# Kernel tuning notes

Measured on AMD Instinct MI355X. Metric: run time of the kernel, lower is better.

Reference implementation:

```python
import jax, jax.numpy as jnp
import numpy as np

EPS_LN = 1e-5
EPS_SUMNORM = 1e-5
B, T, F, H = 8, 1024, 128, 64


def setup_inputs() -> dict:
    key = jax.random.key(0)
    ks = jax.random.split(key, 12)
    s = lambda fan_in: 1.0 / np.sqrt(fan_in)
    inp = {
        "x": jax.random.normal(ks[0], (B, T, F), dtype=jnp.float32),
        "state": jax.random.normal(ks[1], (B, 1, H * H), dtype=jnp.float32),
        # nn.Linear weights are [out, in]
        "Wk": jax.random.uniform(ks[2], (H, F), minval=-s(F), maxval=s(F)),
        "Wq": jax.random.uniform(ks[3], (H, F), minval=-s(F), maxval=s(F)),
        "Wv": jax.random.uniform(ks[4], (H, F), minval=-s(F), maxval=s(F)),
        "gamma": jnp.ones((F,), dtype=jnp.float32),
        "beta": jnp.zeros((F,), dtype=jnp.float32),
        "W1": jax.random.uniform(ks[5], (H, H), minval=-s(H), maxval=s(H)),
        "b1": jax.random.uniform(ks[6], (H,), minval=-s(H), maxval=s(H)),
        "W2": jax.random.uniform(ks[7], (H, H), minval=-s(H), maxval=s(H)),
        "b2": jax.random.uniform(ks[8], (H,), minval=-s(H), maxval=s(H)),
        "Ws": jax.random.uniform(ks[9], (H, F), minval=-s(F), maxval=s(F)),
        "bs": jax.random.uniform(ks[10], (H,), minval=-s(F), maxval=s(F)),
    }
    return inp


def reference(x, state, Wk, Wq, Wv, gamma, beta, W1, b1, W2, b2, Ws, bs):
    # LayerNorm over feature dim
    mu = jnp.mean(x, axis=-1, keepdims=True)
    var = jnp.var(x, axis=-1, keepdims=True)
    xn = (x - mu) * jax.lax.rsqrt(var + EPS_LN) * gamma + beta  # [B,T,F]

    K = jax.nn.relu(jnp.einsum('btf,hf->bth', xn, Wk))
    Q = jax.nn.relu(jnp.einsum('btf,hf->bth', xn, Wq))
    V = jnp.einsum('btf,hf->bth', xn, Wv)

    # sum normalization
    K = K / (EPS_SUMNORM + jnp.sum(K, axis=-1, keepdims=True))
    Q = Q / (EPS_SUMNORM + jnp.sum(Q, axis=-1, keepdims=True))

    # outer-product fast weights: kv[b,t,i,j] = V[b,t,i] * K[b,t,j]
    kv = jnp.einsum('bti,btj->btij', V, K)  # [B,T,H,H]

    # 'sum' aggregator: running sum over time starting from initial state
    S = jnp.cumsum(kv, axis=1) + state.reshape(B, 1, H, H)  # [B,T,H,H]

    y = jnp.einsum('btij,btj->bti', S, Q)  # [B,T,H]

    # feed forward
    y = jax.nn.relu(jnp.einsum('bti,oi->bto', y, W1) + b1)
    y = jax.nn.relu(jnp.einsum('bti,oi->bto', y, W2) + b2)

    # residual shortcut (from the normalized x, matching the torch reassignment)
    y = y + jnp.einsum('btf,hf->bth', xn, Ws) + bs
    return y, S
```

## Files before the change

### kernel.cpp

```cpp
#include <hip/hip_runtime.h>

#define Bn 8
#define Tn 1024
#define Fn 128
#define Hn 64
#define NC 32
#define CSZ 32

constexpr float EPS = 1e-5f;

__device__ __forceinline__ void fma4(float4& a, float s, const float4& w) {
    a.x = fmaf(s, w.x, a.x); a.y = fmaf(s, w.y, a.y);
    a.z = fmaf(s, w.z, a.z); a.w = fmaf(s, w.w, a.w);
}
__device__ __forceinline__ float4 f4zero() { return make_float4(0.f, 0.f, 0.f, 0.f); }

__global__ __launch_bounds__(256) void k_ln(const float* __restrict__ x,
                                            const float* __restrict__ gamma,
                                            const float* __restrict__ beta,
                                            float* __restrict__ xn) {
    const int w = threadIdx.x >> 6, lane = threadIdx.x & 63;
    const int tok = blockIdx.x * 4 + w;
    const float2 xv = *(const float2*)(x + tok * Fn + lane * 2);
    float s  = xv.x + xv.y;
    float ss = xv.x * xv.x + xv.y * xv.y;
#pragma unroll
    for (int m = 1; m < 64; m <<= 1) { s += __shfl_xor(s, m); ss += __shfl_xor(ss, m); }
    const float mu  = s * (1.0f / Fn);
    const float var = ss * (1.0f / Fn) - mu * mu;
    const float rs  = rsqrtf(var + EPS);
    const float2 g  = *(const float2*)(gamma + lane * 2);
    const float2 bt = *(const float2*)(beta + lane * 2);
    float2 o;
    o.x = (xv.x - mu) * rs * g.x + bt.x;
    o.y = (xv.y - mu) * rs * g.y + bt.y;
    *(float2*)(xn + tok * Fn + lane * 2) = o;
}

__global__ __launch_bounds__(256) void k_proj(const float* __restrict__ xn,
                                              const float* __restrict__ Wk,
                                              const float* __restrict__ Wq,
                                              const float* __restrict__ Wv,
                                              const float* __restrict__ Wsp,
                                              const float* __restrict__ bs,
                                              float* __restrict__ Kb, float* __restrict__ Qb,
                                              float* __restrict__ Vb, float* __restrict__ Rb) {
    __shared__ float LW[32 * 260];
    __shared__ float LX[32 * 36];
    const int tid  = threadIdx.x;
    const int tok0 = blockIdx.x * 32;
    const int tg   = tid >> 6;
    const int cg   = tid & 63;

    const int   ms   = tid >> 6;
    const float* WmS = (ms == 0) ? Wk : (ms == 1) ? Wq : (ms == 2) ? Wv : Wsp;
    const float* wrow = WmS + (tid & 63) * Fn;

    float4 acc[8];
#pragma unroll
    for (int i = 0; i < 8; i++) acc[i] = f4zero();

    for (int kc0 = 0; kc0 < Fn; kc0 += 32) {
#pragma unroll
        for (int r = 0; r < 8; r++) {
            const float4 wv = *(const float4*)(wrow + kc0 + r * 4);
            LW[(r * 4 + 0) * 260 + tid] = wv.x;
            LW[(r * 4 + 1) * 260 + tid] = wv.y;
            LW[(r * 4 + 2) * 260 + tid] = wv.z;
            LW[(r * 4 + 3) * 260 + tid] = wv.w;
        }
        {
            const int tt = tid >> 3, kk = (tid & 7) * 4;
            const float4 xv = *(const float4*)(xn + (tok0 + tt) * Fn + kc0 + kk);
            LX[(kk + 0) * 36 + tt] = xv.x;
            LX[(kk + 1) * 36 + tt] = xv.y;
            LX[(kk + 2) * 36 + tt] = xv.z;
            LX[(kk + 3) * 36 + tt] = xv.w;
        }
        __syncthreads();
#pragma unroll 8
        for (int kc = 0; kc < 32; kc++) {
            const float4 w4 = *(const float4*)&LW[kc * 260 + cg * 4];
            const float4 xa = *(const float4*)&LX[kc * 36 + tg * 8];
            const float4 xb = *(const float4*)&LX[kc * 36 + tg * 8 + 4];
            fma4(acc[0], xa.x, w4); fma4(acc[1], xa.y, w4);
            fma4(acc[2], xa.z, w4); fma4(acc[3], xa.w, w4);
            fma4(acc[4], xb.x, w4); fma4(acc[5], xb.y, w4);
            fma4(acc[6], xb.z, w4); fma4(acc[7], xb.w, w4);
        }
        __syncthreads();
    }
    const int m  = cg >> 4;
    const int h0 = (cg & 15) * 4;
    float* outp = (m == 0) ? Kb : (m == 1) ? Qb : (m == 2) ? Vb : Rb;
    if (m < 2) {
#pragma unroll
        for (int i = 0; i < 8; i++) {
            acc[i].x = fmaxf(acc[i].x, 0.f); acc[i].y = fmaxf(acc[i].y, 0.f);
            acc[i].z = fmaxf(acc[i].z, 0.f); acc[i].w = fmaxf(acc[i].w, 0.f);
        }
    } else if (m == 3) {
        const float4 bv = *(const float4*)(bs + h0);
#pragma unroll
        for (int i = 0; i < 8; i++) {
            acc[i].x += bv.x; acc[i].y += bv.y; acc[i].z += bv.z; acc[i].w += bv.w;
        }
    }
#pragma unroll
    for (int ti = 0; ti < 8; ti++)
        *(float4*)(outp + (tok0 + tg * 8 + ti) * Hn + h0) = acc[ti];
}

__global__ __launch_bounds__(256) void k_sumnorm(float* __restrict__ Kb, float* __restrict__ Qb) {
    const int w = threadIdx.x >> 6, lane = threadIdx.x & 63;
    const int tok = blockIdx.x * 2 + (w & 1);
    float* buf = (w >> 1) ? Qb : Kb;
    const float v = buf[tok * Hn + lane];
    float s = v;
#pragma unroll
    for (int m = 1; m < 64; m <<= 1) s += __shfl_xor(s, m);
    buf[tok * Hn + lane] = v / (EPS + s);
}

__global__ __launch_bounds__(256) void k_csum(const float* __restrict__ Kb,
                                              const float* __restrict__ Vb,
                                              float* __restrict__ csum) {
    __shared__ float Kc[CSZ * Hn];
    __shared__ float Vc[CSZ * Hn];
    const int tid = threadIdx.x;
    const int b = blockIdx.x >> 5, c = blockIdx.x & 31;
    const int t0 = c * CSZ;
    const float4* Kg = (const float4*)(Kb + (b * Tn + t0) * Hn);
    const float4* Vg = (const float4*)(Vb + (b * Tn + t0) * Hn);
#pragma unroll
    for (int r = 0; r < 2; r++) {
        ((float4*)Kc)[tid + 256 * r] = Kg[tid + 256 * r];
        ((float4*)Vc)[tid + 256 * r] = Vg[tid + 256 * r];
    }
    __syncthreads();
    float4 acc[4];
#pragma unroll
    for (int s = 0; s < 4; s++) acc[s] = f4zero();
    const int jq = tid & 15, rr = tid >> 4;
    for (int t = 0; t < CSZ; t++) {
        const float4 kv = ((const float4*)Kc)[t * 16 + jq];
#pragma unroll
        for (int s = 0; s < 4; s++) {
            const float v = Vc[t * Hn + s * 16 + rr];
            fma4(acc[s], v, kv);
        }
    }
    float4* out = (float4*)(csum + (size_t)(b * NC + c) * Hn * Hn);
#pragma unroll
    for (int s = 0; s < 4; s++) out[s * 256 + tid] = acc[s];
}

__global__ __launch_bounds__(256) void k_scan(const float* __restrict__ state,
                                              const float* __restrict__ csum,
                                              float* __restrict__ cstart) {
    const int b = blockIdx.x >> 4, et = blockIdx.x & 15;
    const int e = et * 256 + threadIdx.x;
    float v[NC];
#pragma unroll
    for (int c = 0; c < NC; c++) v[c] = csum[(size_t)(b * NC + c) * 4096 + e];
    float acc = state[b * 4096 + e];
#pragma unroll
    for (int c = 0; c < NC; c++) {
        cstart[(size_t)(b * NC + c) * 4096 + e] = acc;
        acc += v[c];
    }
}

__global__ __launch_bounds__(256) void k_main(const float* __restrict__ Kb,
                                              const float* __restrict__ Qb,
                                              const float* __restrict__ Vb,
                                              const float* __restrict__ cstart,
                                              float* __restrict__ yraw,
                                              float* __restrict__ outS) {
    __shared__ float Kc[CSZ * Hn];
    __shared__ float Qc[CSZ * Hn];
    __shared__ float Vc[CSZ * Hn];
    const int tid = threadIdx.x;
    const int b = blockIdx.x >> 5, c = blockIdx.x & 31;
    const int t0 = c * CSZ;
    const float4* Kg = (const float4*)(Kb + (b * Tn + t0) * Hn);
    const float4* Qg = (const float4*)(Qb + (b * Tn + t0) * Hn);
    const float4* Vg = (const float4*)(Vb + (b * Tn + t0) * Hn);
#pragma unroll
    for (int r = 0; r < 2; r++) {
        ((float4*)Kc)[tid + 256 * r] = Kg[tid + 256 * r];
        ((float4*)Qc)[tid + 256 * r] = Qg[tid + 256 * r];
        ((float4*)Vc)[tid + 256 * r] = Vg[tid + 256 * r];
    }
    float4 S4[4];
    const float4* cs = (const float4*)(cstart + (size_t)(b * NC + c) * 4096);
#pragma unroll
    for (int s = 0; s < 4; s++) S4[s] = cs[s * 256 + tid];
    __syncthreads();
    const int jq = tid & 15, rr = tid >> 4;
    float* yBase = yraw + (b * Tn + t0) * Hn;
    float4* SBase = (float4*)outS + (size_t)(b * Tn + t0) * 1024;
    for (int t = 0; t < CSZ; t++) {
        const float4 kv = ((const float4*)Kc)[t * 16 + jq];
        const float4 qv = ((const float4*)Qc)[t * 16 + jq];
        float yp[4];
#pragma unroll
        for (int s = 0; s < 4; s++) {
            const float v = Vc[t * Hn + s * 16 + rr];
            fma4(S4[s], v, kv);
            yp[s] = S4[s].x * qv.x + S4[s].y * qv.y + S4[s].z * qv.z + S4[s].w * qv.w;
        }
        float4* So = SBase + t * 1024;
#pragma unroll
        for (int s = 0; s < 4; s++) So[s * 256 + tid] = S4[s];
#pragma unroll
        for (int s = 0; s < 4; s++) {
            yp[s] += __shfl_xor(yp[s], 1);
            yp[s] += __shfl_xor(yp[s], 2);
            yp[s] += __shfl_xor(yp[s], 4);
            yp[s] += __shfl_xor(yp[s], 8);
        }
        if (jq == 0) {
#pragma unroll
            for (int s = 0; s < 4; s++) yBase[t * Hn + s * 16 + rr] = yp[s];
        }
    }
}

__global__ __launch_bounds__(256) void k_ffn(const float* __restrict__ yraw,
                                             const float* __restrict__ W1,
                                             const float* __restrict__ b1,
                                             const float* __restrict__ W2,
                                             const float* __restrict__ b2,
                                             const float* __restrict__ Rb,
                                             float* __restrict__ outY) {
    __shared__ float WT[2][64 * 68];
    __shared__ float Yt[64 * 36];
    __shared__ float Y2[64 * 36];
    __shared__ float Lb[2][64];
    const int tid = threadIdx.x;
    const int tok0 = blockIdx.x * 32;
    for (int mat = 0; mat < 2; mat++) {
        const float4* Wg = (const float4*)(mat ? W2 : W1);
#pragma unroll
        for (int r = 0; r < 4; r++) {
            const int f4i = tid + 256 * r;
            const float4 wv = Wg[f4i];
            const int h = f4i >> 4;
            const int k = (f4i & 15) * 4;
            WT[mat][(k + 0) * 68 + h] = wv.x;
            WT[mat][(k + 1) * 68 + h] = wv.y;
            WT[mat][(k + 2) * 68 + h] = wv.z;
            WT[mat][(k + 3) * 68 + h] = wv.w;
        }
    }
    if (tid < 64) Lb[0][tid] = b1[tid];
    else if (tid < 128) Lb[1][tid - 64] = b2[tid - 64];
    {
        const float4* Yg = (const float4*)(yraw + tok0 * Hn);
#pragma unroll
        for (int r = 0; r < 2; r++) {
            const int f4i = tid + 256 * r;
            const float4 yv = Yg[f4i];
            const int tok = f4i >> 4;
            const int k = (f4i & 15) * 4;
            Yt[(k + 0) * 36 + tok] = yv.x;
            Yt[(k + 1) * 36 + tok] = yv.y;
            Yt[(k + 2) * 36 + tok] = yv.z;
            Yt[(k + 3) * 36 + tok] = yv.w;
        }
    }
    __syncthreads();
    const int tg = tid >> 4, cg = tid & 15;
    float4 a0 = f4zero(), a1 = f4zero();
#pragma unroll 16
    for (int k = 0; k < 64; k++) {
        const float2 y2 = *(const float2*)&Yt[k * 36 + tg * 2];
        const float4 w4 = *(const float4*)&WT[0][k * 68 + cg * 4];
        fma4(a0, y2.x, w4); fma4(a1, y2.y, w4);
    }
    {
        const float4 bv = *(const float4*)&Lb[0][cg * 4];
        a0.x = fmaxf(a0.x + bv.x, 0.f); a0.y = fmaxf(a0.y + bv.y, 0.f);
        a0.z = fmaxf(a0.z + bv.z, 0.f); a0.w = fmaxf(a0.w + bv.w, 0.f);
        a1.x = fmaxf(a1.x + bv.x, 0.f); a1.y = fmaxf(a1.y + bv.y, 0.f);
        a1.z = fmaxf(a1.z + bv.z, 0.f); a1.w = fmaxf(a1.w + bv.w, 0.f);
    }
    Y2[(cg * 4 + 0) * 36 + tg * 2] = a0.x;
    Y2[(cg * 4 + 1) * 36 + tg * 2] = a0.y;
    Y2[(cg * 4 + 2) * 36 + tg * 2] = a0.z;
    Y2[(cg * 4 + 3) * 36 + tg * 2] = a0.w;
    Y2[(cg * 4 + 0) * 36 + tg * 2 + 1] = a1.x;
    Y2[(cg * 4 + 1) * 36 + tg * 2 + 1] = a1.y;
    Y2[(cg * 4 + 2) * 36 + tg * 2 + 1] = a1.z;
    Y2[(cg * 4 + 3) * 36 + tg * 2 + 1] = a1.w;
    __syncthreads();
    float4 c0 = f4zero(), c1 = f4zero();
#pragma unroll 16
    for (int k = 0; k < 64; k++) {
        const float2 y2 = *(const float2*)&Y2[k * 36 + tg * 2];
        const float4 w4 = *(const float4*)&WT[1][k * 68 + cg * 4];
        fma4(c0, y2.x, w4); fma4(c1, y2.y, w4);
    }
    const int tokA = tok0 + tg * 2, tokB = tokA + 1;
    const float4 bv = *(const float4*)&Lb[1][cg * 4];
    const float4 r0 = *(const float4*)(Rb + tokA * Hn + cg * 4);
    const float4 r1 = *(const float4*)(Rb + tokB * Hn + cg * 4);
    float4 o0, o1;
    o0.x = fmaxf(c0.x + bv.x, 0.f) + r0.x; o0.y = fmaxf(c0.y + bv.y, 0.f) + r0.y;
    o0.z = fmaxf(c0.z + bv.z, 0.f) + r0.z; o0.w = fmaxf(c0.w + bv.w, 0.f) + r0.w;
    o1.x = fmaxf(c1.x + bv.x, 0.f) + r1.x; o1.y = fmaxf(c1.y + bv.y, 0.f) + r1.y;
    o1.z = fmaxf(c1.z + bv.z, 0.f) + r1.z; o1.w = fmaxf(c1.w + bv.w, 0.f) + r1.w;
    *(float4*)(outY + tokA * Hn + cg * 4) = o0;
    *(float4*)(outY + tokB * Hn + cg * 4) = o1;
}

extern "C" void kernel_launch(void* const* d_in, const int* in_sizes, int n_in,
                              void* d_out, int out_size, void* d_ws, size_t ws_size,
                              hipStream_t stream) {
    const float* x     = (const float*)d_in[0];
    const float* state = (const float*)d_in[1];
    const float* Wk    = (const float*)d_in[2];
    const float* Wq    = (const float*)d_in[3];
    const float* Wv    = (const float*)d_in[4];
    const float* gamma = (const float*)d_in[5];
    const float* beta  = (const float*)d_in[6];
    const float* W1    = (const float*)d_in[7];
    const float* b1    = (const float*)d_in[8];
    const float* W2    = (const float*)d_in[9];
    const float* b2    = (const float*)d_in[10];
    const float* Wsp   = (const float*)d_in[11];
    const float* bs    = (const float*)d_in[12];

    float* ws     = (float*)d_ws;
    float* Kb     = ws;
    float* Qb     = ws + 524288;
    float* Vb     = ws + 1048576;
    float* Rb     = ws + 1572864;
    float* yraw   = ws + 2097152;
    float* csum   = ws + 2621440;
    float* cstart = ws + 3670016;
    float* xn     = ws + 4718592;

    float* outY = (float*)d_out;
    float* outS = outY + (size_t)Bn * Tn * Hn;

    k_ln<<<2048, 256, 0, stream>>>(x, gamma, beta, xn);
    k_proj<<<256, 256, 0, stream>>>(xn, Wk, Wq, Wv, Wsp, bs, Kb, Qb, Vb, Rb);
    k_sumnorm<<<4096, 256, 0, stream>>>(Kb, Qb);
    k_csum<<<256, 256, 0, stream>>>(Kb, Vb, csum);
    k_scan<<<128, 256, 0, stream>>>(state, csum, cstart);
    k_main<<<256, 256, 0, stream>>>(Kb, Qb, Vb, cstart, yraw, outS);
    k_ffn<<<256, 256, 0, stream>>>(yraw, W1, b1, W2, b2, Rb, outY);
}
```

Measured before the change: 208.3 us.

## Fuse LayerNorm, sumnorm and chunk sums into projection; fuse FFN into scan-main

Reduces seven kernels to three. LayerNorm is computed in registers inside the projection kernel, and the sum-normalisation and per-chunk KV outer-product sums are folded into its epilogue. The FFN is merged into the main recurrence kernel. Chunk size halves to 16 so the main kernel launches 512 blocks, and the scan writes chunk starts in place. This removes the xn, yraw and cstart round trips and several launches, at the cost of a larger per-thread register array in the scan (64 chunks) and heavier per-block work.

```diff
diff --git a/kernel.cpp b/kernel.cpp
--- a/kernel.cpp
+++ b/kernel.cpp
@@ -4,8 +4,8 @@
 #define Tn 1024
 #define Fn 128
 #define Hn 64
-#define NC 32
-#define CSZ 32
+#define NC 64
+#define CSZ 16
 
 constexpr float EPS = 1e-5f;
 
@@ -15,52 +15,45 @@
 }
 __device__ __forceinline__ float4 f4zero() { return make_float4(0.f, 0.f, 0.f, 0.f); }
 
-__global__ __launch_bounds__(256) void k_ln(const float* __restrict__ x,
-                                            const float* __restrict__ gamma,
-                                            const float* __restrict__ beta,
-                                            float* __restrict__ xn) {
-    const int w = threadIdx.x >> 6, lane = threadIdx.x & 63;
-    const int tok = blockIdx.x * 4 + w;
-    const float2 xv = *(const float2*)(x + tok * Fn + lane * 2);
-    float s  = xv.x + xv.y;
-    float ss = xv.x * xv.x + xv.y * xv.y;
-#pragma unroll
-    for (int m = 1; m < 64; m <<= 1) { s += __shfl_xor(s, m); ss += __shfl_xor(ss, m); }
-    const float mu  = s * (1.0f / Fn);
-    const float var = ss * (1.0f / Fn) - mu * mu;
-    const float rs  = rsqrtf(var + EPS);
-    const float2 g  = *(const float2*)(gamma + lane * 2);
-    const float2 bt = *(const float2*)(beta + lane * 2);
-    float2 o;
-    o.x = (xv.x - mu) * rs * g.x + bt.x;
-    o.y = (xv.y - mu) * rs * g.y + bt.y;
-    *(float2*)(xn + tok * Fn + lane * 2) = o;
-}
-
-__global__ __launch_bounds__(256) void k_proj(const float* __restrict__ xn,
-                                              const float* __restrict__ Wk,
-                                              const float* __restrict__ Wq,
-                                              const float* __restrict__ Wv,
-                                              const float* __restrict__ Wsp,
-                                              const float* __restrict__ bs,
-                                              float* __restrict__ Kb, float* __restrict__ Qb,
-                                              float* __restrict__ Vb, float* __restrict__ Rb) {
+__global__ __launch_bounds__(256) void k1_proj(
+    const float* __restrict__ x, const float* __restrict__ gamma, const float* __restrict__ beta,
+    const float* __restrict__ Wk, const float* __restrict__ Wq, const float* __restrict__ Wv,
+    const float* __restrict__ Wsp, const float* __restrict__ bs,
+    float* __restrict__ Kb, float* __restrict__ Qb, float* __restrict__ Vb, float* __restrict__ Rb,
+    float* __restrict__ csum) {
     __shared__ float LW[32 * 260];
     __shared__ float LX[32 * 36];
+    __shared__ float Kc[32 * Hn];
+    __shared__ float Vc[32 * Hn];
     const int tid  = threadIdx.x;
     const int tok0 = blockIdx.x * 32;
     const int tg   = tid >> 6;
     const int cg   = tid & 63;
 
-    const int   ms   = tid >> 6;
-    const float* WmS = (ms == 0) ? Wk : (ms == 1) ? Wq : (ms == 2) ? Wv : Wsp;
+    const float* WmS  = (tg == 0) ? Wk : (tg == 1) ? Wq : (tg == 2) ? Wv : Wsp;
     const float* wrow = WmS + (tid & 63) * Fn;
 
+    const int tt = tid >> 3, kk = (tid & 7) * 4;
+    float4 xreg[4];
+    float s = 0.f, ss = 0.f;
+#pragma unroll
+    for (int c = 0; c < 4; c++) {
+        xreg[c] = *(const float4*)(x + (tok0 + tt) * Fn + c * 32 + kk);
+        s  += xreg[c].x + xreg[c].y + xreg[c].z + xreg[c].w;
+        ss += xreg[c].x * xreg[c].x + xreg[c].y * xreg[c].y
+            + xreg[c].z * xreg[c].z + xreg[c].w * xreg[c].w;
+    }
+#pragma unroll
+    for (int m = 1; m < 8; m <<= 1) { s += __shfl_xor(s, m); ss += __shfl_xor(ss, m); }
+    const float mu = s * (1.f / Fn);
+    const float rs = rsqrtf(ss * (1.f / Fn) - mu * mu + EPS);
+
     float4 acc[8];
 #pragma unroll
     for (int i = 0; i < 8; i++) acc[i] = f4zero();
 
-    for (int kc0 = 0; kc0 < Fn; kc0 += 32) {
+    for (int c = 0; c < 4; c++) {
+        const int kc0 = c * 32;
 #pragma unroll
         for (int r = 0; r < 8; r++) {
             const float4 wv = *(const float4*)(wrow + kc0 + r * 4);
@@ -70,12 +63,13 @@
             LW[(r * 4 + 3) * 260 + tid] = wv.w;
         }
         {
-            const int tt = tid >> 3, kk = (tid & 7) * 4;
-            const float4 xv = *(const float4*)(xn + (tok0 + tt) * Fn + kc0 + kk);
-            LX[(kk + 0) * 36 + tt] = xv.x;
-            LX[(kk + 1) * 36 + tt] = xv.y;
-            LX[(kk + 2) * 36 + tt] = xv.z;
-            LX[(kk + 3) * 36 + tt] = xv.w;
+            const float4 g4 = *(const float4*)(gamma + kc0 + kk);
+            const float4 b4 = *(const float4*)(beta + kc0 + kk);
+            const float4 xv = xreg[c];
+            LX[(kk + 0) * 36 + tt] = (xv.x - mu) * rs * g4.x + b4.x;
+            LX[(kk + 1) * 36 + tt] = (xv.y - mu) * rs * g4.y + b4.y;
+            LX[(kk + 2) * 36 + tt] = (xv.z - mu) * rs * g4.z + b4.z;
+            LX[(kk + 3) * 36 + tt] = (xv.w - mu) * rs * g4.w + b4.w;
         }
         __syncthreads();
 #pragma unroll 8
@@ -90,15 +84,31 @@
         }
         __syncthreads();
     }
+
     const int m  = cg >> 4;
     const int h0 = (cg & 15) * 4;
-    float* outp = (m == 0) ? Kb : (m == 1) ? Qb : (m == 2) ? Vb : Rb;
     if (m < 2) {
 #pragma unroll
         for (int i = 0; i < 8; i++) {
             acc[i].x = fmaxf(acc[i].x, 0.f); acc[i].y = fmaxf(acc[i].y, 0.f);
             acc[i].z = fmaxf(acc[i].z, 0.f); acc[i].w = fmaxf(acc[i].w, 0.f);
         }
+    }
+    float rsum[8];
+#pragma unroll
+    for (int i = 0; i < 8; i++) {
+        rsum[i] = acc[i].x + acc[i].y + acc[i].z + acc[i].w;
+        rsum[i] += __shfl_xor(rsum[i], 1);
+        rsum[i] += __shfl_xor(rsum[i], 2);
+        rsum[i] += __shfl_xor(rsum[i], 4);
+        rsum[i] += __shfl_xor(rsum[i], 8);
+    }
+    if (m < 2) {
+#pragma unroll
+        for (int i = 0; i < 8; i++) {
+            const float inv = 1.f / (EPS + rsum[i]);
+            acc[i].x *= inv; acc[i].y *= inv; acc[i].z *= inv; acc[i].w *= inv;
+        }
     } else if (m == 3) {
         const float4 bv = *(const float4*)(bs + h0);
 #pragma unroll
@@ -106,58 +116,46 @@
             acc[i].x += bv.x; acc[i].y += bv.y; acc[i].z += bv.z; acc[i].w += bv.w;
         }
     }
+    float* outp = (m == 0) ? Kb : (m == 1) ? Qb : (m == 2) ? Vb : Rb;
 #pragma unroll
     for (int ti = 0; ti < 8; ti++)
         *(float4*)(outp + (tok0 + tg * 8 + ti) * Hn + h0) = acc[ti];
-}
-
-__global__ __launch_bounds__(256) void k_sumnorm(float* __restrict__ Kb, float* __restrict__ Qb) {
-    const int w = threadIdx.x >> 6, lane = threadIdx.x & 63;
-    const int tok = blockIdx.x * 2 + (w & 1);
-    float* buf = (w >> 1) ? Qb : Kb;
-    const float v = buf[tok * Hn + lane];
-    float s = v;
-#pragma unroll
-    for (int m = 1; m < 64; m <<= 1) s += __shfl_xor(s, m);
-    buf[tok * Hn + lane] = v / (EPS + s);
-}
-
-__global__ __launch_bounds__(256) void k_csum(const float* __restrict__ Kb,
-                                              const float* __restrict__ Vb,
-                                              float* __restrict__ csum) {
-    __shared__ float Kc[CSZ * Hn];
-    __shared__ float Vc[CSZ * Hn];
-    const int tid = threadIdx.x;
-    const int b = blockIdx.x >> 5, c = blockIdx.x & 31;
-    const int t0 = c * CSZ;
-    const float4* Kg = (const float4*)(Kb + (b * Tn + t0) * Hn);
-    const float4* Vg = (const float4*)(Vb + (b * Tn + t0) * Hn);
-#pragma unroll
-    for (int r = 0; r < 2; r++) {
-        ((float4*)Kc)[tid + 256 * r] = Kg[tid + 256 * r];
-        ((float4*)Vc)[tid + 256 * r] = Vg[tid + 256 * r];
-    }
-    __syncthreads();
-    float4 acc[4];
-#pragma unroll
-    for (int s = 0; s < 4; s++) acc[s] = f4zero();
+    if (m == 0) {
+#pragma unroll
+        for (int ti = 0; ti < 8; ti++) *(float4*)(Kc + (tg * 8 + ti) * Hn + h0) = acc[ti];
+    } else if (m == 2) {
+#pragma unroll
+        for (int ti = 0; ti < 8; ti++) *(float4*)(Vc + (tg * 8 + ti) * Hn + h0) = acc[ti];
+    }
+    __syncthreads();
+
     const int jq = tid & 15, rr = tid >> 4;
-    for (int t = 0; t < CSZ; t++) {
+    const int b  = tok0 >> 10;
+    const int c0 = ((tok0 & 1023) >> 5) * 2;
+    float4 a4[4];
+    float4* out0 = (float4*)(csum + (size_t)(b * NC + c0) * 4096);
+#pragma unroll
+    for (int sI = 0; sI < 4; sI++) a4[sI] = f4zero();
+    for (int t = 0; t < 16; t++) {
         const float4 kv = ((const float4*)Kc)[t * 16 + jq];
 #pragma unroll
-        for (int s = 0; s < 4; s++) {
-            const float v = Vc[t * Hn + s * 16 + rr];
-            fma4(acc[s], v, kv);
-        }
-    }
-    float4* out = (float4*)(csum + (size_t)(b * NC + c) * Hn * Hn);
-#pragma unroll
-    for (int s = 0; s < 4; s++) out[s * 256 + tid] = acc[s];
-}
-
-__global__ __launch_bounds__(256) void k_scan(const float* __restrict__ state,
-                                              const float* __restrict__ csum,
-                                              float* __restrict__ cstart) {
+        for (int sI = 0; sI < 4; sI++) fma4(a4[sI], Vc[t * Hn + sI * 16 + rr], kv);
+    }
+#pragma unroll
+    for (int sI = 0; sI < 4; sI++) out0[sI * 256 + tid] = a4[sI];
+#pragma unroll
+    for (int sI = 0; sI < 4; sI++) a4[sI] = f4zero();
+    for (int t = 16; t < 32; t++) {
+        const float4 kv = ((const float4*)Kc)[t * 16 + jq];
+#pragma unroll
+        for (int sI = 0; sI < 4; sI++) fma4(a4[sI], Vc[t * Hn + sI * 16 + rr], kv);
+    }
+#pragma unroll
+    for (int sI = 0; sI < 4; sI++) out0[1024 + sI * 256 + tid] = a4[sI];
+}
+
+__global__ __launch_bounds__(256) void k2_scan(const float* __restrict__ state,
+                                               float* __restrict__ csum) {
     const int b = blockIdx.x >> 4, et = blockIdx.x & 15;
     const int e = et * 256 + threadIdx.x;
     float v[NC];
@@ -166,80 +164,31 @@
     float acc = state[b * 4096 + e];
 #pragma unroll
     for (int c = 0; c < NC; c++) {
-        cstart[(size_t)(b * NC + c) * 4096 + e] = acc;
+        csum[(size_t)(b * NC + c) * 4096 + e] = acc;
         acc += v[c];
     }
 }
 
-__global__ __launch_bounds__(256) void k_main(const float* __restrict__ Kb,
-                                              const float* __restrict__ Qb,
-                                              const float* __restrict__ Vb,
-                                              const float* __restrict__ cstart,
-                                              float* __restrict__ yraw,
-                                              float* __restrict__ outS) {
+__global__ __launch_bounds__(256, 2) void k3_main(
+    const float* __restrict__ Kb, const float* __restrict__ Qb, const float* __restrict__ Vb,
+    const float* __restrict__ cstart, const float* __restrict__ Rb,
+    const float* __restrict__ W1, const float* __restrict__ b1,
+    const float* __restrict__ W2, const float* __restrict__ b2,
+    float* __restrict__ outY, float* __restrict__ outS) {
     __shared__ float Kc[CSZ * Hn];
     __shared__ float Qc[CSZ * Hn];
     __shared__ float Vc[CSZ * Hn];
-    const int tid = threadIdx.x;
-    const int b = blockIdx.x >> 5, c = blockIdx.x & 31;
-    const int t0 = c * CSZ;
-    const float4* Kg = (const float4*)(Kb + (b * Tn + t0) * Hn);
-    const float4* Qg = (const float4*)(Qb + (b * Tn + t0) * Hn);
-    const float4* Vg = (const float4*)(Vb + (b * Tn + t0) * Hn);
-#pragma unroll
-    for (int r = 0; r < 2; r++) {
-        ((float4*)Kc)[tid + 256 * r] = Kg[tid + 256 * r];
-        ((float4*)Qc)[tid + 256 * r] = Qg[tid + 256 * r];
-        ((float4*)Vc)[tid + 256 * r] = Vg[tid + 256 * r];
-    }
-    float4 S4[4];
-    const float4* cs = (const float4*)(cstart + (size_t)(b * NC + c) * 4096);
-#pragma unroll
-    for (int s = 0; s < 4; s++) S4[s] = cs[s * 256 + tid];
-    __syncthreads();
-    const int jq = tid & 15, rr = tid >> 4;
-    float* yBase = yraw + (b * Tn + t0) * Hn;
-    float4* SBase = (float4*)outS + (size_t)(b * Tn + t0) * 1024;
-    for (int t = 0; t < CSZ; t++) {
-        const float4 kv = ((const float4*)Kc)[t * 16 + jq];
-        const float4 qv = ((const float4*)Qc)[t * 16 + jq];
-        float yp[4];
-#pragma unroll
-        for (int s = 0; s < 4; s++) {
-            const float v = Vc[t * Hn + s * 16 + rr];
-            fma4(S4[s], v, kv);
-            yp[s] = S4[s].x * qv.x + S4[s].y * qv.y + S4[s].z * qv.z + S4[s].w * qv.w;
-        }
-        float4* So = SBase + t * 1024;
-#pragma unroll
-        for (int s = 0; s < 4; s++) So[s * 256 + tid] = S4[s];
-#pragma unroll
-        for (int s = 0; s < 4; s++) {
-            yp[s] += __shfl_xor(yp[s], 1);
-            yp[s] += __shfl_xor(yp[s], 2);
-            yp[s] += __shfl_xor(yp[s], 4);
-            yp[s] += __shfl_xor(yp[s], 8);
-        }
-        if (jq == 0) {
-#pragma unroll
-            for (int s = 0; s < 4; s++) yBase[t * Hn + s * 16 + rr] = yp[s];
-        }
-    }
-}
-
-__global__ __launch_bounds__(256) void k_ffn(const float* __restrict__ yraw,
-                                             const float* __restrict__ W1,
-                                             const float* __restrict__ b1,
-                                             const float* __restrict__ W2,
-                                             const float* __restrict__ b2,
-                                             const float* __restrict__ Rb,
-                                             float* __restrict__ outY) {
     __shared__ float WT[2][64 * 68];
-    __shared__ float Yt[64 * 36];
-    __shared__ float Y2[64 * 36];
+    __shared__ float Yl[CSZ * 68];
+    __shared__ float Y2[CSZ * 68];
     __shared__ float Lb[2][64];
     const int tid = threadIdx.x;
-    const int tok0 = blockIdx.x * 32;
+    const int b = blockIdx.x >> 6, c = blockIdx.x & 63;
+    const int t0 = c * CSZ;
+    ((float4*)Kc)[tid] = ((const float4*)(Kb + (b * Tn + t0) * Hn))[tid];
+    ((float4*)Qc)[tid] = ((const float4*)(Qb + (b * Tn + t0) * Hn))[tid];
+    ((float4*)Vc)[tid] = ((const float4*)(Vb + (b * Tn + t0) * Hn))[tid];
+#pragma unroll
     for (int mat = 0; mat < 2; mat++) {
         const float4* Wg = (const float4*)(mat ? W2 : W1);
 #pragma unroll
@@ -256,63 +205,56 @@
     }
     if (tid < 64) Lb[0][tid] = b1[tid];
     else if (tid < 128) Lb[1][tid - 64] = b2[tid - 64];
-    {
-        const float4* Yg = (const float4*)(yraw + tok0 * Hn);
-#pragma unroll
-        for (int r = 0; r < 2; r++) {
-            const int f4i = tid + 256 * r;
-            const float4 yv = Yg[f4i];
-            const int tok = f4i >> 4;
-            const int k = (f4i & 15) * 4;
-            Yt[(k + 0) * 36 + tok] = yv.x;
-            Yt[(k + 1) * 36 + tok] = yv.y;
-            Yt[(k + 2) * 36 + tok] = yv.z;
-            Yt[(k + 3) * 36 + tok] = yv.w;
-        }
-    }
-    __syncthreads();
+    float4 S4[4];
+    const float4* cs = (const float4*)(cstart + (size_t)(b * NC + c) * 4096);
+#pragma unroll
+    for (int sI = 0; sI < 4; sI++) S4[sI] = cs[sI * 256 + tid];
+    __syncthreads();
+
+    const int jq = tid & 15, rr = tid >> 4;
+    float4* SBase = (float4*)outS + (size_t)(b * Tn + t0) * 1024;
+    for (int t = 0; t < CSZ; t++) {
+        const float4 kv = ((const float4*)Kc)[t * 16 + jq];
+        const float4 qv = ((const float4*)Qc)[t * 16 + jq];
+        float yp[4];
+#pragma unroll
+        for (int sI = 0; sI < 4; sI++) {
+            fma4(S4[sI], Vc[t * Hn + sI * 16 + rr], kv);
+            yp[sI] = S4[sI].x * qv.x + S4[sI].y * qv.y + S4[sI].z * qv.z + S4[sI].w * qv.w;
+        }
+        float4* So = SBase + t * 1024;
+#pragma unroll
+        for (int sI = 0; sI < 4; sI++) So[sI * 256 + tid] = S4[sI];
+#pragma unroll
+        for (int sI = 0; sI < 4; sI++) {
+            yp[sI] += __shfl_xor(yp[sI], 1);
+            yp[sI] += __shfl_xor(yp[sI], 2);
+            yp[sI] += __shfl_xor(yp[sI], 4);
+            yp[sI] += __shfl_xor(yp[sI], 8);
+        }
+        if (jq == 0) {
+#pragma unroll
+            for (int sI = 0; sI < 4; sI++) Yl[t * 68 + sI * 16 + rr] = yp[sI];
+        }
+    }
+    __syncthreads();
+
     const int tg = tid >> 4, cg = tid & 15;
-    float4 a0 = f4zero(), a1 = f4zero();
+    float4 a = *(const float4*)&Lb[0][cg * 4];
 #pragma unroll 16
-    for (int k = 0; k < 64; k++) {
-        const float2 y2 = *(const float2*)&Yt[k * 36 + tg * 2];
-        const float4 w4 = *(const float4*)&WT[0][k * 68 + cg * 4];
-        fma4(a0, y2.x, w4); fma4(a1, y2.y, w4);
-    }
-    {
-        const float4 bv = *(const float4*)&Lb[0][cg * 4];
-        a0.x = fmaxf(a0.x + bv.x, 0.f); a0.y = fmaxf(a0.y + bv.y, 0.f);
-        a0.z = fmaxf(a0.z + bv.z, 0.f); a0.w = fmaxf(a0.w + bv.w, 0.f);
-        a1.x = fmaxf(a1.x + bv.x, 0.f); a1.y = fmaxf(a1.y + bv.y, 0.f);
-        a1.z = fmaxf(a1.z + bv.z, 0.f); a1.w = fmaxf(a1.w + bv.w, 0.f);
-    }
-    Y2[(cg * 4 + 0) * 36 + tg * 2] = a0.x;
-    Y2[(cg * 4 + 1) * 36 + tg * 2] = a0.y;
-    Y2[(cg * 4 + 2) * 36 + tg * 2] = a0.z;
-    Y2[(cg * 4 + 3) * 36 + tg * 2] = a0.w;
-    Y2[(cg * 4 + 0) * 36 + tg * 2 + 1] = a1.x;
-    Y2[(cg * 4 + 1) * 36 + tg * 2 + 1] = a1.y;
-    Y2[(cg * 4 + 2) * 36 + tg * 2 + 1] = a1.z;
-    Y2[(cg * 4 + 3) * 36 + tg * 2 + 1] = a1.w;
-    __syncthreads();
-    float4 c0 = f4zero(), c1 = f4zero();
+    for (int k = 0; k < 64; k++)
+        fma4(a, Yl[tg * 68 + k], *(const float4*)&WT[0][k * 68 + cg * 4]);
+    a.x = fmaxf(a.x, 0.f); a.y = fmaxf(a.y, 0.f); a.z = fmaxf(a.z, 0.f); a.w = fmaxf(a.w, 0.f);
+    *(float4*)&Y2[tg * 68 + cg * 4] = a;
+    __syncthreads();
+    float4 o = *(const float4*)&Lb[1][cg * 4];
 #pragma unroll 16
-    for (int k = 0; k < 64; k++) {
-        const float2 y2 = *(const float2*)&Y2[k * 36 + tg * 2];
-        const float4 w4 = *(const float4*)&WT[1][k * 68 + cg * 4];
-        fma4(c0, y2.x, w4); fma4(c1, y2.y, w4);
-    }
-    const int tokA = tok0 + tg * 2, tokB = tokA + 1;
-    const float4 bv = *(const float4*)&Lb[1][cg * 4];
-    const float4 r0 = *(const float4*)(Rb + tokA * Hn + cg * 4);
-    const float4 r1 = *(const float4*)(Rb + tokB * Hn + cg * 4);
-    float4 o0, o1;
-    o0.x = fmaxf(c0.x + bv.x, 0.f) + r0.x; o0.y = fmaxf(c0.y + bv.y, 0.f) + r0.y;
-    o0.z = fmaxf(c0.z + bv.z, 0.f) + r0.z; o0.w = fmaxf(c0.w + bv.w, 0.f) + r0.w;
-    o1.x = fmaxf(c1.x + bv.x, 0.f) + r1.x; o1.y = fmaxf(c1.y + bv.y, 0.f) + r1.y;
-    o1.z = fmaxf(c1.z + bv.z, 0.f) + r1.z; o1.w = fmaxf(c1.w + bv.w, 0.f) + r1.w;
-    *(float4*)(outY + tokA * Hn + cg * 4) = o0;
-    *(float4*)(outY + tokB * Hn + cg * 4) = o1;
+    for (int k = 0; k < 64; k++)
+        fma4(o, Y2[tg * 68 + k], *(const float4*)&WT[1][k * 68 + cg * 4]);
+    const float4 r4 = ((const float4*)(Rb + (b * Tn + t0) * Hn))[tid];
+    o.x = fmaxf(o.x, 0.f) + r4.x; o.y = fmaxf(o.y, 0.f) + r4.y;
+    o.z = fmaxf(o.z, 0.f) + r4.z; o.w = fmaxf(o.w, 0.f) + r4.w;
+    ((float4*)(outY + (b * Tn + t0) * Hn))[tid] = o;
 }
 
 extern "C" void kernel_launch(void* const* d_in, const int* in_sizes, int n_in,
@@ -332,24 +274,17 @@
     const float* Wsp   = (const float*)d_in[11];
     const float* bs    = (const float*)d_in[12];
 
-    float* ws     = (float*)d_ws;
-    float* Kb     = ws;
-    float* Qb     = ws + 524288;
-    float* Vb     = ws + 1048576;
-    float* Rb     = ws + 1572864;
-    float* yraw   = ws + 2097152;
-    float* csum   = ws + 2621440;
-    float* cstart = ws + 3670016;
-    float* xn     = ws + 4718592;
+    float* ws   = (float*)d_ws;
+    float* Kb   = ws;
+    float* Qb   = ws + 524288;
+    float* Vb   = ws + 1048576;
+    float* Rb   = ws + 1572864;
+    float* csum = ws + 2097152;
 
     float* outY = (float*)d_out;
     float* outS = outY + (size_t)Bn * Tn * Hn;
 
-    k_ln<<<2048, 256, 0, stream>>>(x, gamma, beta, xn);
-    k_proj<<<256, 256, 0, stream>>>(xn, Wk, Wq, Wv, Wsp, bs, Kb, Qb, Vb, Rb);
-    k_sumnorm<<<4096, 256, 0, stream>>>(Kb, Qb);
-    k_csum<<<256, 256, 0, stream>>>(Kb, Vb, csum);
-    k_scan<<<128, 256, 0, stream>>>(state, csum, cstart);
-    k_main<<<256, 256, 0, stream>>>(Kb, Qb, Vb, cstart, yraw, outS);
-    k_ffn<<<256, 256, 0, stream>>>(yraw, W1, b1, W2, b2, Rb, outY);
-}
+    k1_proj<<<256, 256, 0, stream>>>(x, gamma, beta, Wk, Wq, Wv, Wsp, bs, Kb, Qb, Vb, Rb, csum);
+    k2_scan<<<128, 256, 0, stream>>>(state, csum);
+    k3_main<<<512, 256, 0, stream>>>(Kb, Qb, Vb, csum, Rb, W1, b1, W2, b2, outY, outS);
+}
```

Measured after the change: 194.4 us. 1.07x faster.
